# Performance work log

Hardware: AMD Instinct MI355X
Metric: run time of the kernel (lower is better)

## Reference

```python
import jax, jax.numpy as jnp
import numpy as np

N_NODES = 20000
N_EDGES = 320000
IN_DIM = 128
HID = 64
LATENT = 32
NUM_GRAPHS = 64
NEG_SLOPE = 0.2
BN_EPS = 1e-5


def setup_inputs() -> dict:
    key = jax.random.key(0)
    ks = jax.random.split(key, 24)
    def glorot(k, shape):
        fan_in, fan_out = shape[0], shape[-1]
        lim = (6.0 / (fan_in + fan_out)) ** 0.5
        return jax.random.uniform(k, shape, jnp.float32, -lim, lim)
    inp = {
        "x": jax.random.normal(ks[0], (N_NODES, IN_DIM), jnp.float32),
        "edge_index": jax.random.randint(ks[1], (2, N_EDGES), 0, N_NODES, jnp.int64),
        "batch": jnp.sort(jax.random.randint(ks[2], (N_NODES,), 0, NUM_GRAPHS, jnp.int64)),
        # layer 0: in=128 -> out=64, heads=4
        "Wl0": glorot(ks[3], (IN_DIM, 4 * HID)),
        "Wr0": glorot(ks[4], (IN_DIM, 4 * HID)),
        "att0": glorot(ks[5], (4, HID)),
        "b0": jnp.zeros((4 * HID,), jnp.float32),
        # layer 1: in=256 -> out=64, heads=4
        "Wl1": glorot(ks[6], (4 * HID, 4 * HID)),
        "Wr1": glorot(ks[7], (4 * HID, 4 * HID)),
        "att1": glorot(ks[8], (4, HID)),
        "b1": jnp.zeros((4 * HID,), jnp.float32),
        # layer 2: in=256 -> out=64, heads=1
        "Wl2": glorot(ks[9], (4 * HID, HID)),
        "Wr2": glorot(ks[10], (4 * HID, HID)),
        "att2": glorot(ks[11], (1, HID)),
        "b2": jnp.zeros((HID,), jnp.float32),
        # BatchNorm1d(hidden_dim) in eval mode (running stats)
        "bn_gamma": jax.random.uniform(ks[12], (HID,), jnp.float32, 0.5, 1.5),
        "bn_beta": jax.random.normal(ks[13], (HID,), jnp.float32) * 0.1,
        "bn_mean": jax.random.normal(ks[14], (HID,), jnp.float32) * 0.1,
        "bn_var": jax.random.uniform(ks[15], (HID,), jnp.float32, 0.5, 1.5),
        # fc: hidden -> latent
        "fc_w": glorot(ks[16], (HID, LATENT)),
        "fc_b": jnp.zeros((LATENT,), jnp.float32),
    }
    return inp


def gatv2_layer(h, src, dst, Wl, Wr, att, bias):
    # PyG GATv2Conv (concat=True, negative_slope=0.2, self loops already in src/dst)
    N = h.shape[0]
    H, C = att.shape
    xl = (h @ Wl).reshape(N, H, C)  # source transform
    xr = (h @ Wr).reshape(N, H, C)  # target transform
    e = jax.nn.leaky_relu(xl[src] + xr[dst], NEG_SLOPE)   # [E,H,C]
    logits = jnp.einsum("ehc,hc->eh", e, att)             # [E,H]
    # softmax over incoming edges per destination node
    m = jax.ops.segment_max(logits, dst, num_segments=N)  # [N,H]
    ex = jnp.exp(logits - m[dst])
    denom = jax.ops.segment_sum(ex, dst, num_segments=N)
    alpha = ex / denom[dst]                               # [E,H]
    out = jax.ops.segment_sum(alpha[:, :, None] * xl[src], dst, num_segments=N)
    return out.reshape(N, H * C) + bias


def reference(x, edge_index, batch, Wl0, Wr0, att0, b0, Wl1, Wr1, att1, b1,
              Wl2, Wr2, att2, b2, bn_gamma, bn_beta, bn_mean, bn_var, fc_w, fc_b):
    N = x.shape[0]
    loop = jnp.arange(N, dtype=edge_index.dtype)
    src = jnp.concatenate([edge_index[0], loop])  # add self loops (PyG default)
    dst = jnp.concatenate([edge_index[1], loop])
    h = gatv2_layer(x, src, dst, Wl0, Wr0, att0, b0)   # dropout: eval mode -> identity
    h = gatv2_layer(h, src, dst, Wl1, Wr1, att1, b1)
    h = gatv2_layer(h, src, dst, Wl2, Wr2, att2, b2)   # [N, HID]
    pooled = jax.ops.segment_sum(h, batch, num_segments=NUM_GRAPHS)  # global_add_pool
    bn = (pooled - bn_mean) * jax.lax.rsqrt(bn_var + BN_EPS) * bn_gamma + bn_beta
    return bn @ fc_w + fc_b  # [NUM_GRAPHS, LATENT]
```

## Files before the change

kernel.cpp:

```cpp
#include <hip/hip_runtime.h>
#include <math.h>

#define N_NODES 20000
#define E_ORIG  320000
#define E_TOT   340000
#define NUM_GRAPHS 64
#define NCHUNK 5
#define NBINS (N_NODES * NCHUNK)
#define SCAN_BLOCKS 98

typedef __attribute__((ext_vector_type(8))) short bf16x8;
typedef __attribute__((ext_vector_type(4))) float f32x4;

__device__ __forceinline__ ushort f2bf(float x) {
  unsigned u = __float_as_uint(x);
  return (ushort)((u + 0x7fffu + ((u >> 16) & 1u)) >> 16);
}
__device__ __forceinline__ float4 ld_bf16x4(const ushort* p) {
  ushort4 u = *(const ushort4*)p;
  float4 f;
  f.x = __uint_as_float((unsigned)u.x << 16);
  f.y = __uint_as_float((unsigned)u.y << 16);
  f.z = __uint_as_float((unsigned)u.z << 16);
  f.w = __uint_as_float((unsigned)u.w << 16);
  return f;
}
__device__ __forceinline__ void gl_lds16(const void* g, void* l) {
  __builtin_amdgcn_global_load_lds(
      (const __attribute__((address_space(1))) unsigned*)(uintptr_t)g,
      (__attribute__((address_space(3))) unsigned*)(uintptr_t)l, 16, 0, 0);
}

__global__ __launch_bounds__(256) void prep(
    const float* __restrict__ x,
    const float* __restrict__ Wl0, const float* __restrict__ Wr0,
    const float* __restrict__ Wl1, const float* __restrict__ Wr1,
    const float* __restrict__ Wl2, const float* __restrict__ Wr2,
    ushort* __restrict__ x16, ushort* __restrict__ Bt0,
    ushort* __restrict__ Bt1, ushort* __restrict__ Bt2, int* __restrict__ deg)
{
  const int Z0 = 640000;
  const int Z1 = Z0 + 65536;
  const int Z2 = Z1 + 131072;
  const int Z3 = Z2 + 32768;
  const int Z4 = Z3 + NBINS / 4;
  int t = blockIdx.x * 256 + threadIdx.x;
  if (t < Z0) {
    int i = t << 2;
    float4 v = *(const float4*)&x[i];
    ushort4 o; o.x = f2bf(v.x); o.y = f2bf(v.y); o.z = f2bf(v.z); o.w = f2bf(v.w);
    *(ushort4*)&x16[i] = o;
  } else if (t < Z1) {
    int idx = t - Z0; int n = idx >> 7, k = idx & 127;
    float v = (n < 256) ? Wl0[k * 256 + n] : Wr0[k * 256 + (n - 256)];
    Bt0[idx] = f2bf(v);
  } else if (t < Z2) {
    int idx = t - Z1; int n = idx >> 8, k = idx & 255;
    float v = (n < 256) ? Wl1[k * 256 + n] : Wr1[k * 256 + (n - 256)];
    Bt1[idx] = f2bf(v);
  } else if (t < Z3) {
    int idx = t - Z2; int n = idx >> 8, k = idx & 255;
    float v = (n < 64) ? Wl2[k * 64 + n] : Wr2[k * 64 + (n - 64)];
    Bt2[idx] = f2bf(v);
  } else if (t < Z4) {
    int4 z = {0, 0, 0, 0};
    *(int4*)&deg[(t - Z3) << 2] = z;
  }
}


__global__ __launch_bounds__(256) void deg_count(
    const int* __restrict__ esrc, const int* __restrict__ edst,
    int* __restrict__ deg)
{
  int e = blockIdx.x * 256 + threadIdx.x;
  if (e >= E_TOT) return;
  int src, dst;
  if (e < E_ORIG) { src = esrc[e]; dst = edst[e]; }
  else            { src = dst = e - E_ORIG; }
  atomicAdd(&deg[dst * NCHUNK + (src >> 12)], 1);
}

__global__ __launch_bounds__(256) void scan1(
    const int* __restrict__ deg, int* __restrict__ bsum)
{
  __shared__ int red[256];
  const int t = threadIdx.x;
  int base = (blockIdx.x << 10) + (t << 2);
  int s = 0;
  if (base + 4 <= NBINS) {
    int4 v = *(const int4*)&deg[base];
    s = v.x + v.y + v.z + v.w;
  }
  red[t] = s;
  __syncthreads();
  #pragma unroll
  for (int off = 128; off > 0; off >>= 1) {
    if (t < off) red[t] += red[t + off];
    __syncthreads();
  }
  if (t == 0) bsum[blockIdx.x] = red[0];
}

__global__ __launch_bounds__(256) void scan3(
    const int* __restrict__ deg, const int* __restrict__ bsum,
    int* __restrict__ rowptr, int* __restrict__ cursor)
{
  __shared__ int sc[256];
  __shared__ int bs[128];
  const int t = threadIdx.x;
  if (t < 128) bs[t] = (t < SCAN_BLOCKS) ? bsum[t] : 0;
  __syncthreads();
  #pragma unroll
  for (int off = 1; off < 128; off <<= 1) {
    int v = (t >= off && t < 128) ? bs[t - off] : 0;
    __syncthreads();
    if (t < 128) bs[t] += v;
    __syncthreads();
  }
  const int myoff = (blockIdx.x == 0) ? 0 : bs[blockIdx.x - 1];

  int base = (blockIdx.x << 10) + (t << 2);
  int4 v = {0, 0, 0, 0};
  if (base + 4 <= NBINS) v = *(const int4*)&deg[base];
  int s = v.x + v.y + v.z + v.w;
  sc[t] = s;
  __syncthreads();
  #pragma unroll
  for (int off = 1; off < 256; off <<= 1) {
    int u = (t >= off) ? sc[t - off] : 0;
    __syncthreads();
    sc[t] += u;
    __syncthreads();
  }
  if (base + 4 <= NBINS) {
    int p = myoff + ((t == 0) ? 0 : sc[t - 1]);
    int4 r;
    r.x = p; r.y = p + v.x; r.z = r.y + v.y; r.w = r.z + v.z;
    *(int4*)&rowptr[base] = r;
    *(int4*)&cursor[base] = r;
  }
  if (blockIdx.x == SCAN_BLOCKS - 1 && t == 255) rowptr[NBINS] = bs[127];
}

__global__ __launch_bounds__(256) void csr_fill(
    const int* __restrict__ esrc, const int* __restrict__ edst,
    int* __restrict__ cursor, int* __restrict__ csr_src)
{
  int e = blockIdx.x * 256 + threadIdx.x;
  if (e >= E_TOT) return;
  int src, dst;
  if (e < E_ORIG) { src = esrc[e]; dst = edst[e]; }
  else            { src = dst = e - E_ORIG; }
  int pos = atomicAdd(&cursor[dst * NCHUNK + (src >> 12)], 1);
  csr_src[pos] = src;
}

__global__ __launch_bounds__(256) void mfma_gemm_bf16(
    const ushort* __restrict__ A, const ushort* __restrict__ Bt,
    ushort* __restrict__ C, int M, int K, int N)
{
  __shared__ char smem[36864];
  ushort* As = (ushort*)smem;
  ushort* Bs = As + 8192;

  const int mtiles = (M + 127) >> 7;
  const int bid = blockIdx.x;
  const int xcd = bid & 7;
  const int i = bid >> 3;
  const int n0 = (i / 20) << 7;
  const int m = xcd + ((i % 20) << 3);
  if (m >= mtiles) return;
  const int m0 = m << 7;

  const int tid = threadIdx.x;
  const int lane = tid & 63;
  const int w = tid >> 6;
  const int wm = (w >> 1) << 6;
  const int wn = (w & 1) << 6;
  const int quad = lane >> 4;
  const int l15 = lane & 15;

  f32x4 acc[4][4] = {};

  for (int k0 = 0; k0 < K; k0 += 64) {
    #pragma unroll
    for (int r = 0; r < 4; r++) {
      int c = (r << 8) + tid;
      int row = c >> 3;
      int col = (c & 7) << 3;
      int ga = m0 + row; if (ga >= M) ga = M - 1;
      gl_lds16(A  + (size_t)ga * K + k0 + col, (char*)As + c * 16);
      gl_lds16(Bt + (size_t)(n0 + row) * K + k0 + col, (char*)Bs + c * 16);
    }
    __syncthreads();
    #pragma unroll
    for (int ks = 0; ks < 2; ks++) {
      bf16x8 af[4], bfr[4];
      #pragma unroll
      for (int ii = 0; ii < 4; ii++)
        af[ii]  = *(const bf16x8*)&As[(wm + (ii << 4) + l15) * 64 + (ks << 5) + (quad << 3)];
      #pragma unroll
      for (int j = 0; j < 4; j++)
        bfr[j] = *(const bf16x8*)&Bs[(wn + (j << 4) + l15) * 64 + (ks << 5) + (quad << 3)];
      #pragma unroll
      for (int ii = 0; ii < 4; ii++)
        #pragma unroll
        for (int j = 0; j < 4; j++)
          acc[ii][j] = __builtin_amdgcn_mfma_f32_16x16x32_bf16(
              af[ii], bfr[j], acc[ii][j], 0, 0, 0);
    }
    __syncthreads();
  }

  ushort* Cs = (ushort*)smem + w * 4608;
  #pragma unroll
  for (int ii = 0; ii < 4; ii++)
    #pragma unroll
    for (int j = 0; j < 4; j++)
      #pragma unroll
      for (int r = 0; r < 4; r++)
        Cs[((ii << 4) + (quad << 2) + r) * 72 + (j << 4) + l15] = f2bf(acc[ii][j][r]);
  #pragma unroll
  for (int it = 0; it < 8; it++) {
    int row = (it << 3) + (lane >> 3);
    int cc = lane & 7;
    bf16x8 v = *(const bf16x8*)&Cs[row * 72 + (cc << 3)];
    int grow = m0 + wm + row;
    if (grow < M)
      *(bf16x8*)&C[(size_t)grow * N + n0 + wn + (cc << 3)] = v;
  }
}

__device__ __forceinline__ void h4_term(
    float4 xlv, const float4& xrv, const float4& attv, float& v)
{
  float4 a;
  a.x = xlv.x + xrv.x; a.y = xlv.y + xrv.y;
  a.z = xlv.z + xrv.z; a.w = xlv.w + xrv.w;
  a.x = fmaxf(a.x, 0.2f * a.x); a.y = fmaxf(a.y, 0.2f * a.y);
  a.z = fmaxf(a.z, 0.2f * a.z); a.w = fmaxf(a.w, 0.2f * a.w);
  v = a.x * attv.x + a.y * attv.y + a.z * attv.z + a.w * attv.w;
}

__device__ __forceinline__ void h4_edge(
    const float4& xv, const float4& xrv, const float4& attv,
    float4& acc, float& lsum)
{
  float v;
  h4_term(xv, xrv, attv, v);
  v += __shfl_xor(v, 1);
  v += __shfl_xor(v, 2);
  v += __shfl_xor(v, 4);
  v += __shfl_xor(v, 8);
  float w = __expf(v);
  lsum += w;
  acc.x += w * xv.x; acc.y += w * xv.y;
  acc.z += w * xv.z; acc.w += w * xv.w;
}

__global__ __launch_bounds__(256) void gat_gather_h4(
    const ushort* __restrict__ Cin, const float* __restrict__ att,
    const float* __restrict__ bias, const int* __restrict__ rowptr,
    const int* __restrict__ csr_src, ushort* __restrict__ hout)
{
  const int n = blockIdx.x * 4 + (threadIdx.x >> 6);
  const int lane = threadIdx.x & 63;
  const int c4 = lane << 2;
  const float4 xrv  = ld_bf16x4(Cin + (size_t)n * 512 + 256 + c4);
  const float4 attv = *(const float4*)&att[c4];
  const int beg = rowptr[n * NCHUNK], end = rowptr[n * NCHUNK + NCHUNK];
  float4 acc = make_float4(0.f, 0.f, 0.f, 0.f);
  float lsum = 0.f;
  int p = beg;
  for (; p + 7 < end; p += 8) {
    int s0 = csr_src[p],     s1 = csr_src[p + 1];
    int s2 = csr_src[p + 2], s3 = csr_src[p + 3];
    int s4 = csr_src[p + 4], s5 = csr_src[p + 5];
    int s6 = csr_src[p + 6], s7 = csr_src[p + 7];
    float4 x0 = ld_bf16x4(Cin + (size_t)s0 * 512 + c4);
    float4 x1 = ld_bf16x4(Cin + (size_t)s1 * 512 + c4);
    float4 x2 = ld_bf16x4(Cin + (size_t)s2 * 512 + c4);
    float4 x3 = ld_bf16x4(Cin + (size_t)s3 * 512 + c4);
    float4 x4 = ld_bf16x4(Cin + (size_t)s4 * 512 + c4);
    float4 x5 = ld_bf16x4(Cin + (size_t)s5 * 512 + c4);
    float4 x6 = ld_bf16x4(Cin + (size_t)s6 * 512 + c4);
    float4 x7 = ld_bf16x4(Cin + (size_t)s7 * 512 + c4);
    h4_edge(x0, xrv, attv, acc, lsum);
    h4_edge(x1, xrv, attv, acc, lsum);
    h4_edge(x2, xrv, attv, acc, lsum);
    h4_edge(x3, xrv, attv, acc, lsum);
    h4_edge(x4, xrv, attv, acc, lsum);
    h4_edge(x5, xrv, attv, acc, lsum);
    h4_edge(x6, xrv, attv, acc, lsum);
    h4_edge(x7, xrv, attv, acc, lsum);
  }
  for (; p + 3 < end; p += 4) {
    int s0 = csr_src[p],     s1 = csr_src[p + 1];
    int s2 = csr_src[p + 2], s3 = csr_src[p + 3];
    float4 x0 = ld_bf16x4(Cin + (size_t)s0 * 512 + c4);
    float4 x1 = ld_bf16x4(Cin + (size_t)s1 * 512 + c4);
    float4 x2 = ld_bf16x4(Cin + (size_t)s2 * 512 + c4);
    float4 x3 = ld_bf16x4(Cin + (size_t)s3 * 512 + c4);
    h4_edge(x0, xrv, attv, acc, lsum);
    h4_edge(x1, xrv, attv, acc, lsum);
    h4_edge(x2, xrv, attv, acc, lsum);
    h4_edge(x3, xrv, attv, acc, lsum);
  }
  for (; p < end; p++) {
    int s0 = csr_src[p];
    float4 x0 = ld_bf16x4(Cin + (size_t)s0 * 512 + c4);
    h4_edge(x0, xrv, attv, acc, lsum);
  }
  const float4 bv = *(const float4*)&bias[c4];
  float inv = 1.f / lsum;
  ushort4 o;
  o.x = f2bf(acc.x * inv + bv.x); o.y = f2bf(acc.y * inv + bv.y);
  o.z = f2bf(acc.z * inv + bv.z); o.w = f2bf(acc.w * inv + bv.w);
  *(ushort4*)&hout[(size_t)n * 256 + c4] = o;
}

__global__ __launch_bounds__(256) void gat_gather_h1(
    const ushort* __restrict__ Cin, const float* __restrict__ att,
    const float* __restrict__ bias, const int* __restrict__ rowptr,
    const int* __restrict__ csr_src, float* __restrict__ h3)
{
  const int n = blockIdx.x * 4 + (threadIdx.x >> 6);
  const int lane = threadIdx.x & 63;
  const int g = lane >> 4, c4 = (lane & 15) << 2;
  const float4 xrv  = ld_bf16x4(Cin + (size_t)n * 128 + 64 + c4);
  const float4 attv = *(const float4*)&att[c4];
  const int beg = rowptr[n * NCHUNK], end = rowptr[n * NCHUNK + NCHUNK];
  float4 acc = make_float4(0.f, 0.f, 0.f, 0.f);
  float lsum = 0.f;
  int p = beg + g;
  for (; p + 4 < end; p += 8) {
    int s0 = csr_src[p], s1 = csr_src[p + 4];
    float4 x0 = ld_bf16x4(Cin + (size_t)s0 * 128 + c4);
    float4 x1 = ld_bf16x4(Cin + (size_t)s1 * 128 + c4);
    h4_edge(x0, xrv, attv, acc, lsum);
    h4_edge(x1, xrv, attv, acc, lsum);
  }
  if (p < end) {
    int s0 = csr_src[p];
    float4 x0 = ld_bf16x4(Cin + (size_t)s0 * 128 + c4);
    h4_edge(x0, xrv, attv, acc, lsum);
  }
  #pragma unroll
  for (int off = 16; off <= 32; off <<= 1) {
    lsum  += __shfl_xor(lsum, off);
    acc.x += __shfl_xor(acc.x, off); acc.y += __shfl_xor(acc.y, off);
    acc.z += __shfl_xor(acc.z, off); acc.w += __shfl_xor(acc.w, off);
  }
  if (g == 0) {
    const float4 bv = *(const float4*)&bias[c4];
    float inv = 1.f / lsum;
    float4 o;
    o.x = acc.x * inv + bv.x; o.y = acc.y * inv + bv.y;
    o.z = acc.z * inv + bv.z; o.w = acc.w * inv + bv.w;
    *(float4*)&h3[(size_t)n * 64 + c4] = o;
  }
}

__global__ __launch_bounds__(256) void pool_bn_fc(
    const float* __restrict__ h3, const int* __restrict__ batch,
    const float* __restrict__ gamma, const float* __restrict__ beta,
    const float* __restrict__ mean, const float* __restrict__ var,
    const float* __restrict__ fcw, const float* __restrict__ fcb,
    float* __restrict__ out)
{
  __shared__ float red[256];
  __shared__ float s[64];
  const int g = blockIdx.x;
  const int t = threadIdx.x;
  const int c = t & 63, r = t >> 6;
  int lo = 0, hi = N_NODES;
  while (lo < hi) { int mid = (lo + hi) >> 1; if (batch[mid] < g) lo = mid + 1; else hi = mid; }
  int s0 = lo;
  hi = N_NODES;
  while (lo < hi) { int mid = (lo + hi) >> 1; if (batch[mid] < g + 1) lo = mid + 1; else hi = mid; }
  int e0 = lo;
  float a = 0.f;
  for (int n = s0 + r; n < e0; n += 4) a += h3[(size_t)n * 64 + c];
  red[t] = a;
  __syncthreads();
  if (r == 0) {
    float p = red[c] + red[c + 64] + red[c + 128] + red[c + 192];
    s[c] = (p - mean[c]) * rsqrtf(var[c] + 1e-5f) * gamma[c] + beta[c];
  }
  __syncthreads();
  if (t < 32) {
    float acc = fcb[t];
    #pragma unroll
    for (int k = 0; k < 64; k++) acc += s[k] * fcw[k * 32 + t];
    out[g * 32 + t] = acc;
  }
}

extern "C" void kernel_launch(void* const* d_in, const int* in_sizes, int n_in,
                              void* d_out, int out_size, void* d_ws, size_t ws_size,
                              hipStream_t stream) {
  const float* x    = (const float*)d_in[0];
  const int*   ei   = (const int*)d_in[1];
  const int*   batch= (const int*)d_in[2];
  const float* Wl0  = (const float*)d_in[3];
  const float* Wr0  = (const float*)d_in[4];
  const float* att0 = (const float*)d_in[5];
  const float* b0   = (const float*)d_in[6];
  const float* Wl1  = (const float*)d_in[7];
  const float* Wr1  = (const float*)d_in[8];
  const float* att1 = (const float*)d_in[9];
  const float* b1   = (const float*)d_in[10];
  const float* Wl2  = (const float*)d_in[11];
  const float* Wr2  = (const float*)d_in[12];
  const float* att2 = (const float*)d_in[13];
  const float* b2   = (const float*)d_in[14];
  const float* bng  = (const float*)d_in[15];
  const float* bnb  = (const float*)d_in[16];
  const float* bnm  = (const float*)d_in[17];
  const float* bnv  = (const float*)d_in[18];
  const float* fcw  = (const float*)d_in[19];
  const float* fcb  = (const float*)d_in[20];
  float* out = (float*)d_out;

  const int* esrc = ei;
  const int* edst = ei + E_ORIG;

  char* w = (char*)d_ws;
  ushort* x16  = (ushort*)w;                 w += (size_t)N_NODES * 128 * 2;
  ushort* Cbig = (ushort*)w;                 w += (size_t)N_NODES * 512 * 2;
  ushort* h16  = (ushort*)w;                 w += (size_t)N_NODES * 256 * 2;
  ushort* C2   = (ushort*)w;                 w += (size_t)N_NODES * 128 * 2;
  float*  h3   = (float*)w;                  w += (size_t)N_NODES * 64 * 4;
  ushort* Bt0  = (ushort*)w;                 w += (size_t)512 * 128 * 2;
  ushort* Bt1  = (ushort*)w;                 w += (size_t)512 * 256 * 2;
  ushort* Bt2  = (ushort*)w;                 w += (size_t)128 * 256 * 2;
  int* deg     = (int*)w;                    w += NBINS * 4;
  int* rowptr  = (int*)w;                    w += (NBINS + 1) * 4;
  int* cursor  = (int*)w;                    w += NBINS * 4;
  int* bsum    = (int*)w;                    w += 128 * 4;
  int* csr_src = (int*)w;

  dim3 blk(256);
  const int eblk = (E_TOT + 255) / 256;

  prep<<<dim3(3495), blk, 0, stream>>>(
      x, Wl0, Wr0, Wl1, Wr1, Wl2, Wr2, x16, Bt0, Bt1, Bt2, deg);

  deg_count<<<dim3(eblk), blk, 0, stream>>>(esrc, edst, deg);
  scan1<<<dim3(SCAN_BLOCKS), blk, 0, stream>>>(deg, bsum);
  scan3<<<dim3(SCAN_BLOCKS), blk, 0, stream>>>(deg, bsum, rowptr, cursor);
  csr_fill<<<dim3(eblk), blk, 0, stream>>>(esrc, edst, cursor, csr_src);

  mfma_gemm_bf16<<<dim3(160 * 4), blk, 0, stream>>>(x16, Bt0, Cbig, N_NODES, 128, 512);
  gat_gather_h4<<<dim3(N_NODES / 4), blk, 0, stream>>>(
      Cbig, att0, b0, rowptr, csr_src, h16);

  mfma_gemm_bf16<<<dim3(160 * 4), blk, 0, stream>>>(h16, Bt1, Cbig, N_NODES, 256, 512);
  gat_gather_h4<<<dim3(N_NODES / 4), blk, 0, stream>>>(
      Cbig, att1, b1, rowptr, csr_src, h16);

  mfma_gemm_bf16<<<dim3(160 * 1), blk, 0, stream>>>(h16, Bt2, C2, N_NODES, 256, 128);
  gat_gather_h1<<<dim3(N_NODES / 4), blk, 0, stream>>>(
      C2, att2, b2, rowptr, csr_src, h3);

  pool_bn_fc<<<dim3(NUM_GRAPHS), blk, 0, stream>>>(
      h3, batch, bng, bnb, bnm, bnv, fcw, fcb, out);
}
```

Measured before the change: 286.0 us.

## Split GEMM output into separate xl/xr buffers and refine CSR source chunks

```diff
diff --git a/kernel.cpp b/kernel.cpp
--- a/kernel.cpp
+++ b/kernel.cpp
@@ -5,9 +5,9 @@
 #define E_ORIG  320000
 #define E_TOT   340000
 #define NUM_GRAPHS 64
-#define NCHUNK 5
+#define NCHUNK 10
 #define NBINS (N_NODES * NCHUNK)
-#define SCAN_BLOCKS 98
+#define SCAN_BLOCKS 196
 
 typedef __attribute__((ext_vector_type(8))) short bf16x8;
 typedef __attribute__((ext_vector_type(4))) float f32x4;
@@ -78,7 +78,7 @@
   int src, dst;
   if (e < E_ORIG) { src = esrc[e]; dst = edst[e]; }
   else            { src = dst = e - E_ORIG; }
-  atomicAdd(&deg[dst * NCHUNK + (src >> 12)], 1);
+  atomicAdd(&deg[dst * NCHUNK + (src >> 11)], 1);
 }
 
 __global__ __launch_bounds__(256) void scan1(
@@ -107,15 +107,15 @@
     int* __restrict__ rowptr, int* __restrict__ cursor)
 {
   __shared__ int sc[256];
-  __shared__ int bs[128];
+  __shared__ int bs[256];
   const int t = threadIdx.x;
-  if (t < 128) bs[t] = (t < SCAN_BLOCKS) ? bsum[t] : 0;
+  bs[t] = (t < SCAN_BLOCKS) ? bsum[t] : 0;
   __syncthreads();
   #pragma unroll
-  for (int off = 1; off < 128; off <<= 1) {
-    int v = (t >= off && t < 128) ? bs[t - off] : 0;
-    __syncthreads();
-    if (t < 128) bs[t] += v;
+  for (int off = 1; off < 256; off <<= 1) {
+    int v = (t >= off) ? bs[t - off] : 0;
+    __syncthreads();
+    bs[t] += v;
     __syncthreads();
   }
   const int myoff = (blockIdx.x == 0) ? 0 : bs[blockIdx.x - 1];
@@ -140,7 +140,7 @@
     *(int4*)&rowptr[base] = r;
     *(int4*)&cursor[base] = r;
   }
-  if (blockIdx.x == SCAN_BLOCKS - 1 && t == 255) rowptr[NBINS] = bs[127];
+  if (blockIdx.x == SCAN_BLOCKS - 1 && t == 255) rowptr[NBINS] = bs[255];
 }
 
 __global__ __launch_bounds__(256) void csr_fill(
@@ -152,13 +152,13 @@
   int src, dst;
   if (e < E_ORIG) { src = esrc[e]; dst = edst[e]; }
   else            { src = dst = e - E_ORIG; }
-  int pos = atomicAdd(&cursor[dst * NCHUNK + (src >> 12)], 1);
+  int pos = atomicAdd(&cursor[dst * NCHUNK + (src >> 11)], 1);
   csr_src[pos] = src;
 }
 
 __global__ __launch_bounds__(256) void mfma_gemm_bf16(
     const ushort* __restrict__ A, const ushort* __restrict__ Bt,
-    ushort* __restrict__ C, int M, int K, int N)
+    ushort* __restrict__ Cl, ushort* __restrict__ Cr, int M, int K, int N)
 {
   __shared__ char smem[36864];
   ushort* As = (ushort*)smem;
@@ -213,6 +213,11 @@
     __syncthreads();
   }
 
+  const int halfN = N >> 1;
+  const int gc0 = n0 + wn;
+  ushort* Cd = (gc0 < halfN) ? Cl : Cr;
+  const int cb = (gc0 < halfN) ? gc0 : gc0 - halfN;
+
   ushort* Cs = (ushort*)smem + w * 4608;
   #pragma unroll
   for (int ii = 0; ii < 4; ii++)
@@ -228,7 +233,7 @@
     bf16x8 v = *(const bf16x8*)&Cs[row * 72 + (cc << 3)];
     int grow = m0 + wm + row;
     if (grow < M)
-      *(bf16x8*)&C[(size_t)grow * N + n0 + wn + (cc << 3)] = v;
+      *(bf16x8*)&Cd[(size_t)grow * halfN + cb + (cc << 3)] = v;
   }
 }
 
@@ -260,14 +265,15 @@
 }
 
 __global__ __launch_bounds__(256) void gat_gather_h4(
-    const ushort* __restrict__ Cin, const float* __restrict__ att,
-    const float* __restrict__ bias, const int* __restrict__ rowptr,
-    const int* __restrict__ csr_src, ushort* __restrict__ hout)
+    const ushort* __restrict__ xl16, const ushort* __restrict__ xr16,
+    const float* __restrict__ att, const float* __restrict__ bias,
+    const int* __restrict__ rowptr, const int* __restrict__ csr_src,
+    ushort* __restrict__ hout)
 {
   const int n = blockIdx.x * 4 + (threadIdx.x >> 6);
   const int lane = threadIdx.x & 63;
   const int c4 = lane << 2;
-  const float4 xrv  = ld_bf16x4(Cin + (size_t)n * 512 + 256 + c4);
+  const float4 xrv  = ld_bf16x4(xr16 + (size_t)n * 256 + c4);
   const float4 attv = *(const float4*)&att[c4];
   const int beg = rowptr[n * NCHUNK], end = rowptr[n * NCHUNK + NCHUNK];
   float4 acc = make_float4(0.f, 0.f, 0.f, 0.f);
@@ -278,14 +284,14 @@
     int s2 = csr_src[p + 2], s3 = csr_src[p + 3];
     int s4 = csr_src[p + 4], s5 = csr_src[p + 5];
     int s6 = csr_src[p + 6], s7 = csr_src[p + 7];
-    float4 x0 = ld_bf16x4(Cin + (size_t)s0 * 512 + c4);
-    float4 x1 = ld_bf16x4(Cin + (size_t)s1 * 512 + c4);
-    float4 x2 = ld_bf16x4(Cin + (size_t)s2 * 512 + c4);
-    float4 x3 = ld_bf16x4(Cin + (size_t)s3 * 512 + c4);
-    float4 x4 = ld_bf16x4(Cin + (size_t)s4 * 512 + c4);
-    float4 x5 = ld_bf16x4(Cin + (size_t)s5 * 512 + c4);
-    float4 x6 = ld_bf16x4(Cin + (size_t)s6 * 512 + c4);
-    float4 x7 = ld_bf16x4(Cin + (size_t)s7 * 512 + c4);
+    float4 x0 = ld_bf16x4(xl16 + (size_t)s0 * 256 + c4);
+    float4 x1 = ld_bf16x4(xl16 + (size_t)s1 * 256 + c4);
+    float4 x2 = ld_bf16x4(xl16 + (size_t)s2 * 256 + c4);
+    float4 x3 = ld_bf16x4(xl16 + (size_t)s3 * 256 + c4);
+    float4 x4 = ld_bf16x4(xl16 + (size_t)s4 * 256 + c4);
+    float4 x5 = ld_bf16x4(xl16 + (size_t)s5 * 256 + c4);
+    float4 x6 = ld_bf16x4(xl16 + (size_t)s6 * 256 + c4);
+    float4 x7 = ld_bf16x4(xl16 + (size_t)s7 * 256 + c4);
     h4_edge(x0, xrv, attv, acc, lsum);
     h4_edge(x1, xrv, attv, acc, lsum);
     h4_edge(x2, xrv, attv, acc, lsum);
@@ -298,10 +304,10 @@
   for (; p + 3 < end; p += 4) {
     int s0 = csr_src[p],     s1 = csr_src[p + 1];
     int s2 = csr_src[p + 2], s3 = csr_src[p + 3];
-    float4 x0 = ld_bf16x4(Cin + (size_t)s0 * 512 + c4);
-    float4 x1 = ld_bf16x4(Cin + (size_t)s1 * 512 + c4);
-    float4 x2 = ld_bf16x4(Cin + (size_t)s2 * 512 + c4);
-    float4 x3 = ld_bf16x4(Cin + (size_t)s3 * 512 + c4);
+    float4 x0 = ld_bf16x4(xl16 + (size_t)s0 * 256 + c4);
+    float4 x1 = ld_bf16x4(xl16 + (size_t)s1 * 256 + c4);
+    float4 x2 = ld_bf16x4(xl16 + (size_t)s2 * 256 + c4);
+    float4 x3 = ld_bf16x4(xl16 + (size_t)s3 * 256 + c4);
     h4_edge(x0, xrv, attv, acc, lsum);
     h4_edge(x1, xrv, attv, acc, lsum);
     h4_edge(x2, xrv, attv, acc, lsum);
@@ -309,7 +315,7 @@
   }
   for (; p < end; p++) {
     int s0 = csr_src[p];
-    float4 x0 = ld_bf16x4(Cin + (size_t)s0 * 512 + c4);
+    float4 x0 = ld_bf16x4(xl16 + (size_t)s0 * 256 + c4);
     h4_edge(x0, xrv, attv, acc, lsum);
   }
   const float4 bv = *(const float4*)&bias[c4];
@@ -321,14 +327,15 @@
 }
 
 __global__ __launch_bounds__(256) void gat_gather_h1(
-    const ushort* __restrict__ Cin, const float* __restrict__ att,
-    const float* __restrict__ bias, const int* __restrict__ rowptr,
-    const int* __restrict__ csr_src, float* __restrict__ h3)
+    const ushort* __restrict__ xl2, const ushort* __restrict__ xr2,
+    const float* __restrict__ att, const float* __restrict__ bias,
+    const int* __restrict__ rowptr, const int* __restrict__ csr_src,
+    float* __restrict__ h3)
 {
   const int n = blockIdx.x * 4 + (threadIdx.x >> 6);
   const int lane = threadIdx.x & 63;
   const int g = lane >> 4, c4 = (lane & 15) << 2;
-  const float4 xrv  = ld_bf16x4(Cin + (size_t)n * 128 + 64 + c4);
+  const float4 xrv  = ld_bf16x4(xr2 + (size_t)n * 64 + c4);
   const float4 attv = *(const float4*)&att[c4];
   const int beg = rowptr[n * NCHUNK], end = rowptr[n * NCHUNK + NCHUNK];
   float4 acc = make_float4(0.f, 0.f, 0.f, 0.f);
@@ -336,14 +343,14 @@
   int p = beg + g;
   for (; p + 4 < end; p += 8) {
     int s0 = csr_src[p], s1 = csr_src[p + 4];
-    float4 x0 = ld_bf16x4(Cin + (size_t)s0 * 128 + c4);
-    float4 x1 = ld_bf16x4(Cin + (size_t)s1 * 128 + c4);
+    float4 x0 = ld_bf16x4(xl2 + (size_t)s0 * 64 + c4);
+    float4 x1 = ld_bf16x4(xl2 + (size_t)s1 * 64 + c4);
     h4_edge(x0, xrv, attv, acc, lsum);
     h4_edge(x1, xrv, attv, acc, lsum);
   }
   if (p < end) {
     int s0 = csr_src[p];
-    float4 x0 = ld_bf16x4(Cin + (size_t)s0 * 128 + c4);
+    float4 x0 = ld_bf16x4(xl2 + (size_t)s0 * 64 + c4);
     h4_edge(x0, xrv, attv, acc, lsum);
   }
   #pragma unroll
@@ -428,9 +435,11 @@
 
   char* w = (char*)d_ws;
   ushort* x16  = (ushort*)w;                 w += (size_t)N_NODES * 128 * 2;
-  ushort* Cbig = (ushort*)w;                 w += (size_t)N_NODES * 512 * 2;
   ushort* h16  = (ushort*)w;                 w += (size_t)N_NODES * 256 * 2;
-  ushort* C2   = (ushort*)w;                 w += (size_t)N_NODES * 128 * 2;
+  ushort* xl16 = (ushort*)w;                 w += (size_t)N_NODES * 256 * 2;
+  ushort* xr16 = (ushort*)w;                 w += (size_t)N_NODES * 256 * 2;
+  ushort* xl2  = (ushort*)w;                 w += (size_t)N_NODES * 64 * 2;
+  ushort* xr2  = (ushort*)w;                 w += (size_t)N_NODES * 64 * 2;
   float*  h3   = (float*)w;                  w += (size_t)N_NODES * 64 * 4;
   ushort* Bt0  = (ushort*)w;                 w += (size_t)512 * 128 * 2;
   ushort* Bt1  = (ushort*)w;                 w += (size_t)512 * 256 * 2;
@@ -438,13 +447,13 @@
   int* deg     = (int*)w;                    w += NBINS * 4;
   int* rowptr  = (int*)w;                    w += (NBINS + 1) * 4;
   int* cursor  = (int*)w;                    w += NBINS * 4;
-  int* bsum    = (int*)w;                    w += 128 * 4;
+  int* bsum    = (int*)w;                    w += 256 * 4;
   int* csr_src = (int*)w;
 
   dim3 blk(256);
   const int eblk = (E_TOT + 255) / 256;
 
-  prep<<<dim3(3495), blk, 0, stream>>>(
+  prep<<<dim3(3592), blk, 0, stream>>>(
       x, Wl0, Wr0, Wl1, Wr1, Wl2, Wr2, x16, Bt0, Bt1, Bt2, deg);
 
   deg_count<<<dim3(eblk), blk, 0, stream>>>(esrc, edst, deg);
@@ -452,17 +461,20 @@
   scan3<<<dim3(SCAN_BLOCKS), blk, 0, stream>>>(deg, bsum, rowptr, cursor);
   csr_fill<<<dim3(eblk), blk, 0, stream>>>(esrc, edst, cursor, csr_src);
 
-  mfma_gemm_bf16<<<dim3(160 * 4), blk, 0, stream>>>(x16, Bt0, Cbig, N_NODES, 128, 512);
+  mfma_gemm_bf16<<<dim3(160 * 4), blk, 0, stream>>>(
+      x16, Bt0, xl16, xr16, N_NODES, 128, 512);
   gat_gather_h4<<<dim3(N_NODES / 4), blk, 0, stream>>>(
-      Cbig, att0, b0, rowptr, csr_src, h16);
-
-  mfma_gemm_bf16<<<dim3(160 * 4), blk, 0, stream>>>(h16, Bt1, Cbig, N_NODES, 256, 512);
+      xl16, xr16, att0, b0, rowptr, csr_src, h16);
+
+  mfma_gemm_bf16<<<dim3(160 * 4), blk, 0, stream>>>(
+      h16, Bt1, xl16, xr16, N_NODES, 256, 512);
   gat_gather_h4<<<dim3(N_NODES / 4), blk, 0, stream>>>(
-      Cbig, att1, b1, rowptr, csr_src, h16);
-
-  mfma_gemm_bf16<<<dim3(160 * 1), blk, 0, stream>>>(h16, Bt2, C2, N_NODES, 256, 128);
+      xl16, xr16, att1, b1, rowptr, csr_src, h16);
+
+  mfma_gemm_bf16<<<dim3(160 * 1), blk, 0, stream>>>(
+      h16, Bt2, xl2, xr2, N_NODES, 256, 128);
   gat_gather_h1<<<dim3(N_NODES / 4), blk, 0, stream>>>(
-      C2, att2, b2, rowptr, csr_src, h3);
+      xl2, xr2, att2, b2, rowptr, csr_src, h3);
 
   pool_bn_fc<<<dim3(NUM_GRAPHS), blk, 0, stream>>>(
       h3, batch, bng, bnb, bnm, bnv, fcw, fcb, out);
```

Result: no change. 287.6 us (+0.6%).
